# Kernel optimization log

Hardware: AMD Instinct MI355X
Metric: run time of the kernel (lower is better)

Reference implementation:

```python
import jax, jax.numpy as jnp
import numpy as np
from functools import partial


def edt_sq(mask):
    """Exact squared Euclidean distance transform (distance from True pixels to
    nearest False pixel), separable two-pass algorithm. mask: bool (..., H, W).
    Matches scipy.ndimage.distance_transform_edt(mask)**2 whenever each 2-D
    slice contains at least one background (False) pixel."""
    H, W = mask.shape[-2], mask.shape[-1]
    LARGE = jnp.float32(H * H + W * W + 1)

    # ---- pass 1: 1-D distance to nearest False along H (rows axis) ----
    mm = jnp.moveaxis(mask, -2, 0)  # (H, ..., W)
    init = jnp.full(mm.shape[1:], LARGE, dtype=jnp.float32)

    def step1(carry, x):
        d = jnp.where(x, carry + 1.0, 0.0)
        return d, d

    _, fwd = jax.lax.scan(step1, init, mm)
    _, bwd = jax.lax.scan(step1, init, mm[::-1])
    d1 = jnp.minimum(fwd, bwd[::-1])            # (H, ..., W) 1-D distance
    f = jnp.minimum(d1 * d1, LARGE)             # squared, capped
    f = jnp.moveaxis(f, 0, -2)                  # (..., H, W)

    # ---- pass 2: D[..., j] = min_k f[..., k] + (j - k)^2 along W ----
    j = jnp.arange(W, dtype=jnp.float32)
    fT = jnp.moveaxis(f, -1, 0)                 # (W, ..., H)

    def step2(D, xk):
        fk, k = xk                               # fk: (..., H)
        cand = fk[..., None] + (j - k) ** 2      # (..., H, W)
        return jnp.minimum(D, cand), None

    D0 = jnp.full(f.shape, LARGE, dtype=jnp.float32)
    D, _ = jax.lax.scan(step2, D0, (fT, j))
    return D


def setup_inputs() -> dict:
    key = jax.random.key(0)
    k1, k2 = jax.random.split(key)
    output = jax.random.normal(k1, (16, 2, 512, 512), dtype=jnp.float32)
    target = jax.random.randint(k2, (16, 512, 512), 0, 2).astype(jnp.int64)
    return {"output": output, "target": target}


def reference(output, target):
    B, C, H, W = output.shape
    probs = jax.nn.softmax(output, axis=1)                    # (B,C,H,W)
    y_onehot = jax.nn.one_hot(target, C, axis=1, dtype=jnp.float32)

    # distance maps only needed for channels 1: (loop starts at c=1)
    pc_mask = probs[:, 1:] > 0.5                              # (B,C-1,H,W)
    gt_mask = y_onehot[:, 1:] > 0.5
    pc_dist_sq = edt_sq(pc_mask)
    gt_dist_sq = edt_sq(gt_mask)
    dist = jax.lax.stop_gradient(pc_dist_sq + gt_dist_sq)     # no_grad in torch

    pred_error = (probs - y_onehot) ** 2                      # (B,C,H,W)
    multipled = pred_error[:, 1:] * dist                      # einsum 'bcxy,bcxy->bcxy'
    return multipled.mean()
```

## Files before the change

### kernel.cpp

```cpp
#include <hip/hip_runtime.h>

#define BB   16
#define HH   512
#define WW   512
#define HWSZ (HH * WW)
#define NPIX (BB * HWSZ)
#define LARGE_F 524289.0f
#define NW 16
#define GR 8
#define NLOSSBLK (BB * HH / GR)


__global__ __launch_bounds__(512) void pack_kernel(
    const float* __restrict__ out4,
    const int* __restrict__ target,
    unsigned int* __restrict__ bitsG,
    float* __restrict__ eG) {
  __shared__ unsigned char mbyte[32 * 256];

  const int w    = blockIdx.x >> 1;
  const int half = blockIdx.x & 1;
  const int b    = blockIdx.y;
  const int c0   = half * 256;
  const float* ch0 = out4 + (size_t)(b * 2) * HWSZ;
  const float* ch1 = ch0 + HWSZ;
  const int* tb = target + (size_t)b * HWSZ;
  float* eb = eG + (size_t)b * HWSZ;

#pragma unroll
  for (int s = 0; s < 4; ++s) {
    int q  = s * 512 + threadIdx.x;
    int i  = q >> 6;
    int cq = (q & 63) * 4;
    int g  = (w * 32 + i) * WW + c0 + cq;
    float4 a0 = *(const float4*)(ch0 + g);
    float4 a1 = *(const float4*)(ch1 + g);
    int4   t4 = *(const int4*)(tb + g);
    unsigned p = 0;
    p |= (unsigned)(((a1.x > a0.x) ? 1u : 0u) | ((t4.x == 1) ? 2u : 0u));
    p |= (unsigned)(((a1.y > a0.y) ? 1u : 0u) | ((t4.y == 1) ? 2u : 0u)) << 8;
    p |= (unsigned)(((a1.z > a0.z) ? 1u : 0u) | ((t4.z == 1) ? 2u : 0u)) << 16;
    p |= (unsigned)(((a1.w > a0.w) ? 1u : 0u) | ((t4.w == 1) ? 2u : 0u)) << 24;
    *(unsigned*)&mbyte[i * 256 + cq] = p;

    float4 e4;
    {
      float p1 = 1.0f / (1.0f + expf(a0.x - a1.x));
      float d  = p1 - ((t4.x == 1) ? 1.0f : 0.0f);
      e4.x = d * d;
    }
    {
      float p1 = 1.0f / (1.0f + expf(a0.y - a1.y));
      float d  = p1 - ((t4.y == 1) ? 1.0f : 0.0f);
      e4.y = d * d;
    }
    {
      float p1 = 1.0f / (1.0f + expf(a0.z - a1.z));
      float d  = p1 - ((t4.z == 1) ? 1.0f : 0.0f);
      e4.z = d * d;
    }
    {
      float p1 = 1.0f / (1.0f + expf(a0.w - a1.w));
      float d  = p1 - ((t4.w == 1) ? 1.0f : 0.0f);
      e4.w = d * d;
    }
    *(float4*)(eb + g) = e4;
  }
  __syncthreads();

  {
    int c   = threadIdx.x & 255;
    int sel = threadIdx.x >> 8;
    unsigned wd = 0;
#pragma unroll
    for (int k = 0; k < 32; ++k) {
      unsigned mb = mbyte[k * 256 + c];
      wd |= ((mb >> sel) & 1u) << k;
    }
    bitsG[(size_t)((b * 2 + sel) * NW + w) * WW + c0 + c] = wd;
  }
}

__device__ __forceinline__ int colprobe(const unsigned (*lb)[WW],
                                        const unsigned* __restrict__ gcol,
                                        int wlo, int whi, int j, int i) {
  int w = i >> 5, bp = i & 31;
  unsigned cur = lb[w - wlo][j];
  unsigned zu = ~cur & (0xFFFFFFFFu >> (31 - bp));
  unsigned zd = ~cur & (0xFFFFFFFFu << bp);
  int up = 0xFFFF, dn = 0xFFFF;
  if (zu) {
    up = bp - (31 - __clz(zu));
  } else {
    for (int ww = w - 1; ww >= 0; --ww) {
      unsigned z = ~((ww >= wlo) ? lb[ww - wlo][j] : gcol[ww * WW]);
      if (z) { up = i - (ww * 32 + 31 - __clz(z)); break; }
    }
  }
  if (zd) {
    dn = (__ffs((int)zd) - 1) - bp;
  } else {
    for (int ww = w + 1; ww < NW; ++ww) {
      unsigned z = ~((ww <= whi) ? lb[ww - wlo][j] : gcol[ww * WW]);
      if (z) { dn = ww * 32 + (__ffs((int)z) - 1) - i; break; }
    }
  }
  return min(min(up, dn), 0xFFFF);
}

__global__ __launch_bounds__(512) void loss_kernel(
    const float* __restrict__ eG,
    const unsigned int* __restrict__ bitsG,
    float* __restrict__ partials) {
  __shared__ unsigned lbits[2][5][WW];
  __shared__ float2 fv[GR][WW];
  __shared__ float ssum[8];

  const int b  = blockIdx.x >> 6;
  const int i0 = (blockIdx.x & 63) * GR;
  const int j  = threadIdx.x;

  const int wc  = i0 >> 5;
  const int wlo = max(0, wc - 2);
  const int whi = min(NW - 1, wc + 2);
  const int nwr = whi - wlo + 1;

  const unsigned* gb = bitsG + (size_t)(b * 2) * NW * WW;
  for (int idx = threadIdx.x; idx < nwr * 2 * WW; idx += 512) {
    int c    = idx & (WW - 1);
    int rest = idx >> 9;
    int wrel = rest >> 1;
    int sel  = rest & 1;
    lbits[sel][wrel][c] = gb[(size_t)(sel * NW + wlo + wrel) * WW + c];
  }

  const float* ep = eG + (size_t)b * HWSZ + (size_t)i0 * WW;
  float ev[GR];
#pragma unroll
  for (int rw = 0; rw < GR; ++rw) ev[rw] = ep[rw * WW + j];
  __syncthreads();

  const unsigned* gpc = gb + j;
  const unsigned* ggt = gb + NW * WW + j;
  float bpc[GR], bgt[GR];
#pragma unroll
  for (int rw = 0; rw < GR; ++rw) {
    int i = i0 + rw;
    int rpc = colprobe(lbits[0], gpc, wlo, whi, j, i);
    int rgt = colprobe(lbits[1], ggt, wlo, whi, j, i);
    float fpc = (rpc >= 512) ? LARGE_F : (float)(rpc * rpc);
    float fgt = (rgt >= 512) ? LARGE_F : (float)(rgt * rgt);
    fv[rw][j] = make_float2(fpc, fgt);
    bpc[rw] = fpc; bgt[rw] = fgt;
  }
  __syncthreads();

  for (int r = 1; r < WW; ++r) {
    float rr = (float)(r * r);
    float mx = 0.0f;
#pragma unroll
    for (int rw = 0; rw < GR; ++rw) mx = fmaxf(mx, fmaxf(bpc[rw], bgt[rw]));
    if (rr >= mx) break;
    int jl = j - r, jr = j + r;
    if (jl >= 0) {
#pragma unroll
      for (int rw = 0; rw < GR; ++rw) {
        float2 a = fv[rw][jl];
        bpc[rw] = fminf(bpc[rw], a.x + rr);
        bgt[rw] = fminf(bgt[rw], a.y + rr);
      }
    }
    if (jr < WW) {
#pragma unroll
      for (int rw = 0; rw < GR; ++rw) {
        float2 a = fv[rw][jr];
        bpc[rw] = fminf(bpc[rw], a.x + rr);
        bgt[rw] = fminf(bgt[rw], a.y + rr);
      }
    }
  }

  float contrib = 0.0f;
#pragma unroll
  for (int rw = 0; rw < GR; ++rw) contrib += ev[rw] * (bpc[rw] + bgt[rw]);
  contrib *= (1.0f / (float)NPIX);

  for (int off = 32; off > 0; off >>= 1) contrib += __shfl_down(contrib, off);
  int lane = threadIdx.x & 63;
  int wave = threadIdx.x >> 6;
  if (lane == 0) ssum[wave] = contrib;
  __syncthreads();
  if (threadIdx.x == 0) {
    float s = 0.0f;
#pragma unroll
    for (int w = 0; w < 8; ++w) s += ssum[w];
    partials[blockIdx.x] = s;
  }
}

__global__ __launch_bounds__(1024) void reduce_kernel(
    const float* __restrict__ partials, float* __restrict__ d_out) {
  __shared__ float ssum[16];
  float s = partials[threadIdx.x];
  for (int off = 32; off > 0; off >>= 1) s += __shfl_down(s, off);
  int lane = threadIdx.x & 63;
  int wave = threadIdx.x >> 6;
  if (lane == 0) ssum[wave] = s;
  __syncthreads();
  if (threadIdx.x == 0) {
    float t = 0.0f;
#pragma unroll
    for (int w = 0; w < 16; ++w) t += ssum[w];
    *d_out = t;
  }
}

extern "C" void kernel_launch(void* const* d_in, const int* in_sizes, int n_in,
                              void* d_out, int out_size, void* d_ws, size_t ws_size,
                              hipStream_t stream) {
  const float* out4 = (const float*)d_in[0];
  const int* target = (const int*)d_in[1];
  unsigned int* bitsG = (unsigned int*)d_ws;
  float* eG = (float*)(bitsG + BB * 2 * NW * WW);
  float* partials = eG + NPIX;
  float* out = (float*)d_out;

  dim3 grid1(32, BB);
  pack_kernel<<<grid1, 512, 0, stream>>>(out4, target, bitsG, eG);

  loss_kernel<<<NLOSSBLK, 512, 0, stream>>>(eG, bitsG, partials);

  reduce_kernel<<<1, 1024, 0, stream>>>(partials, out);
}
```

Baseline: 104.7 us.

## Store squared error in fp16 and batch column probes across row group

The per-pixel squared prediction error buffer is now stored as half precision, halving its write and read traffic between the pack and loss kernels. The column distance probe now runs once per 8-row group, finding the nearest zero above the first row and below the last row, then propagating run lengths through the 8 bits in registers instead of probing each row separately. This cuts the shared-memory and bit-scan work of the vertical pass, but fp16 rounding of the error term slightly perturbs the final mean.

```diff
diff --git a/kernel.cpp b/kernel.cpp
--- a/kernel.cpp
+++ b/kernel.cpp
@@ -1,4 +1,5 @@
 #include <hip/hip_runtime.h>
+#include <hip/hip_fp16.h>
 
 #define BB   16
 #define HH   512
@@ -15,7 +16,7 @@
     const float* __restrict__ out4,
     const int* __restrict__ target,
     unsigned int* __restrict__ bitsG,
-    float* __restrict__ eG) {
+    __half* __restrict__ eG) {
   __shared__ unsigned char mbyte[32 * 256];
 
   const int w    = blockIdx.x >> 1;
@@ -25,7 +26,7 @@
   const float* ch0 = out4 + (size_t)(b * 2) * HWSZ;
   const float* ch1 = ch0 + HWSZ;
   const int* tb = target + (size_t)b * HWSZ;
-  float* eb = eG + (size_t)b * HWSZ;
+  __half* eb = eG + (size_t)b * HWSZ;
 
 #pragma unroll
   for (int s = 0; s < 4; ++s) {
@@ -43,28 +44,15 @@
     p |= (unsigned)(((a1.w > a0.w) ? 1u : 0u) | ((t4.w == 1) ? 2u : 0u)) << 24;
     *(unsigned*)&mbyte[i * 256 + cq] = p;
 
-    float4 e4;
-    {
-      float p1 = 1.0f / (1.0f + expf(a0.x - a1.x));
-      float d  = p1 - ((t4.x == 1) ? 1.0f : 0.0f);
-      e4.x = d * d;
-    }
-    {
-      float p1 = 1.0f / (1.0f + expf(a0.y - a1.y));
-      float d  = p1 - ((t4.y == 1) ? 1.0f : 0.0f);
-      e4.y = d * d;
-    }
-    {
-      float p1 = 1.0f / (1.0f + expf(a0.z - a1.z));
-      float d  = p1 - ((t4.z == 1) ? 1.0f : 0.0f);
-      e4.z = d * d;
-    }
-    {
-      float p1 = 1.0f / (1.0f + expf(a0.w - a1.w));
-      float d  = p1 - ((t4.w == 1) ? 1.0f : 0.0f);
-      e4.w = d * d;
-    }
-    *(float4*)(eb + g) = e4;
+    float d0, d1, d2, d3;
+    d0 = 1.0f / (1.0f + expf(a0.x - a1.x)) - ((t4.x == 1) ? 1.0f : 0.0f);
+    d1 = 1.0f / (1.0f + expf(a0.y - a1.y)) - ((t4.y == 1) ? 1.0f : 0.0f);
+    d2 = 1.0f / (1.0f + expf(a0.z - a1.z)) - ((t4.z == 1) ? 1.0f : 0.0f);
+    d3 = 1.0f / (1.0f + expf(a0.w - a1.w)) - ((t4.w == 1) ? 1.0f : 0.0f);
+    __half2 e01 = __floats2half2_rn(d0 * d0, d1 * d1);
+    __half2 e23 = __floats2half2_rn(d2 * d2, d3 * d3);
+    *(__half2*)(eb + g)     = e01;
+    *(__half2*)(eb + g + 2) = e23;
   }
   __syncthreads();
 
@@ -81,35 +69,49 @@
   }
 }
 
-__device__ __forceinline__ int colprobe(const unsigned (*lb)[WW],
-                                        const unsigned* __restrict__ gcol,
-                                        int wlo, int whi, int j, int i) {
-  int w = i >> 5, bp = i & 31;
-  unsigned cur = lb[w - wlo][j];
+__device__ __forceinline__ void colprobe8(const unsigned (*lb)[WW],
+                                          const unsigned* __restrict__ gcol,
+                                          int wlo, int whi, int j, int i0,
+                                          int* __restrict__ rr) {
+  const int w = i0 >> 5, bp = i0 & 31;
+  const unsigned cur = lb[w - wlo][j];
+
   unsigned zu = ~cur & (0xFFFFFFFFu >> (31 - bp));
-  unsigned zd = ~cur & (0xFFFFFFFFu << bp);
-  int up = 0xFFFF, dn = 0xFFFF;
+  int up = 0xFFFF;
   if (zu) {
     up = bp - (31 - __clz(zu));
   } else {
     for (int ww = w - 1; ww >= 0; --ww) {
       unsigned z = ~((ww >= wlo) ? lb[ww - wlo][j] : gcol[ww * WW]);
-      if (z) { up = i - (ww * 32 + 31 - __clz(z)); break; }
-    }
-  }
+      if (z) { up = i0 - (ww * 32 + 31 - __clz(z)); break; }
+    }
+  }
+  const int bp7 = bp + 7;
+  unsigned zd = ~cur & (0xFFFFFFFFu << bp7);
+  int dn = 0xFFFF;
   if (zd) {
-    dn = (__ffs((int)zd) - 1) - bp;
+    dn = (__ffs((int)zd) - 1) - bp7;
   } else {
     for (int ww = w + 1; ww < NW; ++ww) {
       unsigned z = ~((ww <= whi) ? lb[ww - wlo][j] : gcol[ww * WW]);
-      if (z) { dn = ww * 32 + (__ffs((int)z) - 1) - i; break; }
-    }
-  }
-  return min(min(up, dn), 0xFFFF);
+      if (z) { dn = ww * 32 + (__ffs((int)z) - 1) - (i0 + 7); break; }
+    }
+  }
+
+  const unsigned bits8 = (cur >> bp) & 0xFFu;
+  int ups[GR], dns[GR];
+  ups[0] = up;
+  for (int k = 1; k < GR; ++k)
+    ups[k] = ((bits8 >> k) & 1u) ? ups[k - 1] + 1 : 0;
+  dns[GR - 1] = dn;
+  for (int k = GR - 2; k >= 0; --k)
+    dns[k] = ((bits8 >> k) & 1u) ? dns[k + 1] + 1 : 0;
+#pragma unroll
+  for (int k = 0; k < GR; ++k) rr[k] = min(ups[k], dns[k]);
 }
 
 __global__ __launch_bounds__(512) void loss_kernel(
-    const float* __restrict__ eG,
+    const __half* __restrict__ eG,
     const unsigned int* __restrict__ bitsG,
     float* __restrict__ partials) {
   __shared__ unsigned lbits[2][5][WW];
@@ -134,22 +136,23 @@
     lbits[sel][wrel][c] = gb[(size_t)(sel * NW + wlo + wrel) * WW + c];
   }
 
-  const float* ep = eG + (size_t)b * HWSZ + (size_t)i0 * WW;
+  const __half* ep = eG + (size_t)b * HWSZ + (size_t)i0 * WW;
   float ev[GR];
 #pragma unroll
-  for (int rw = 0; rw < GR; ++rw) ev[rw] = ep[rw * WW + j];
+  for (int rw = 0; rw < GR; ++rw) ev[rw] = __half2float(ep[rw * WW + j]);
   __syncthreads();
 
   const unsigned* gpc = gb + j;
   const unsigned* ggt = gb + NW * WW + j;
+  int rpc[GR], rgt[GR];
+  colprobe8(lbits[0], gpc, wlo, whi, j, i0, rpc);
+  colprobe8(lbits[1], ggt, wlo, whi, j, i0, rgt);
+
   float bpc[GR], bgt[GR];
 #pragma unroll
   for (int rw = 0; rw < GR; ++rw) {
-    int i = i0 + rw;
-    int rpc = colprobe(lbits[0], gpc, wlo, whi, j, i);
-    int rgt = colprobe(lbits[1], ggt, wlo, whi, j, i);
-    float fpc = (rpc >= 512) ? LARGE_F : (float)(rpc * rpc);
-    float fgt = (rgt >= 512) ? LARGE_F : (float)(rgt * rgt);
+    float fpc = (rpc[rw] >= 512) ? LARGE_F : (float)(rpc[rw] * rpc[rw]);
+    float fgt = (rgt[rw] >= 512) ? LARGE_F : (float)(rgt[rw] * rgt[rw]);
     fv[rw][j] = make_float2(fpc, fgt);
     bpc[rw] = fpc; bgt[rw] = fgt;
   }
@@ -221,8 +224,8 @@
   const float* out4 = (const float*)d_in[0];
   const int* target = (const int*)d_in[1];
   unsigned int* bitsG = (unsigned int*)d_ws;
-  float* eG = (float*)(bitsG + BB * 2 * NW * WW);
-  float* partials = eG + NPIX;
+  __half* eG = (__half*)(bitsG + BB * 2 * NW * WW);
+  float* partials = (float*)(eG + NPIX);
   float* out = (float*)d_out;
 
   dim3 grid1(32, BB);
```

Result: faster. 95.95 us (-8.3%).
